# Kernel tuning notes

Measured on AMD Instinct MI355X. Metric: run time of the kernel, lower is better.

Reference implementation:

```python
import jax, jax.numpy as jnp
import numpy as np

NEG_INF = -1e30  # masked_softmax fill (squad util convention)


def setup_inputs() -> dict:
    key = jax.random.key(0)
    ks = jax.random.split(key, 5)
    B, S, H = 4, 2048, 512
    x = jax.random.normal(ks[0], (B, S, H), dtype=jnp.float32)
    mask = jax.random.randint(ks[1], (B, S), 0, 2, dtype=jnp.int32)
    mask = mask.at[:, 0].set(1)  # ensure at least one valid key per row
    W_comb = jax.random.normal(ks[2], (H, 3 * H), dtype=jnp.float32) * (1.0 / np.sqrt(H))
    b_comb = jnp.zeros((3 * H,), dtype=jnp.float32)
    W_out = jax.random.normal(ks[3], (H, H), dtype=jnp.float32) * (1.0 / np.sqrt(H))
    b_out = jnp.zeros((H,), dtype=jnp.float32)
    return {"x": x, "mask": mask, "W_comb": W_comb, "b_comb": b_comb,
            "W_out": W_out, "b_out": b_out}


def reference(x, mask, W_comb, b_comb, W_out, b_out):
    B, S, H = x.shape
    n_head = 8
    d = H // n_head
    scale = d ** 0.5
    qkv = x @ W_comb + b_comb                      # [B,S,3H]
    q, k, v = jnp.split(qkv, 3, axis=-1)
    q = q.reshape(B, S, n_head, d)
    k = k.reshape(B, S, n_head, d)
    v = v.reshape(B, S, n_head, d)
    # [B,h,Sq,Sk] scores; mask applies along the key axis
    scores = jnp.einsum('bqhd,bkhd->bhqk', q / scale, k)
    key_mask = (mask > 0)[:, None, None, :]        # [B,1,1,Sk]
    logits = jnp.where(key_mask, scores, NEG_INF)
    attn = jax.nn.softmax(logits, axis=-1)         # dropout = identity (eval)
    out = jnp.einsum('bhqk,bkhd->bqhd', attn, v).reshape(B, S, H)
    return out @ W_out + b_out
```

## Files before the change

### kernel.cpp

```cpp
#include <hip/hip_runtime.h>
#include <hip/hip_bf16.h>
#include <stdint.h>

typedef unsigned short u16;
typedef unsigned int u32;
typedef __attribute__((ext_vector_type(8))) __bf16 bf16x8;
typedef __attribute__((ext_vector_type(8))) unsigned short us8;
typedef __attribute__((ext_vector_type(4))) unsigned short us4;
typedef __attribute__((ext_vector_type(4))) float f32x4;
typedef __attribute__((ext_vector_type(16))) float f32x16;
typedef __attribute__((ext_vector_type(4))) unsigned int u32x4;
typedef __attribute__((ext_vector_type(2))) unsigned int u32x2;

#define KSCALE_Q 0.18033688011112042f

__device__ inline u16 f2bf(float f) {
  union { __bf16 b; u16 s; } x; x.b = (__bf16)f; return x.s;
}
__device__ inline u32 packbf(float a, float b) {
  return (u32)f2bf(a) | ((u32)f2bf(b) << 16);
}
__device__ inline f32x16 zero16() {
  f32x16 z; for (int i = 0; i < 16; ++i) z[i] = 0.f; return z;
}
__device__ __forceinline__ void gl_lds16(const u16* g, u16* l) {
  __builtin_amdgcn_global_load_lds(
      (const __attribute__((address_space(1))) void*)g,
      (__attribute__((address_space(3))) void*)l, 16, 0, 0);
}
__device__ __forceinline__ void pl32swap(u32& a, u32& b) {
#if __has_builtin(__builtin_amdgcn_permlane32_swap)
  u32x2 r = __builtin_amdgcn_permlane32_swap(a, b, false, false);
  a = r[0]; b = r[1];
#else
  u32 ta = (u32)__shfl_xor((int)a, 32);
  u32 tb = (u32)__shfl_xor((int)b, 32);
  int hi = (threadIdx.x & 63) >> 5;
  u32 na = hi ? tb : a;
  u32 nb = hi ? b : ta;
  a = na; b = nb;
#endif
}

__global__ __launch_bounds__(256) void prep(
    const float* __restrict__ x, const float* __restrict__ Wc,
    const float* __restrict__ Wo, const int* __restrict__ mask,
    u16* __restrict__ xbf, u16* __restrict__ wct, u16* __restrict__ wot,
    int* __restrict__ idx, int* __restrict__ nbv) {
  int r = blockIdx.x, tid = threadIdx.x;
  if (r < 4096) {
    int i = r * 256 + tid;
    float4 v = ((const float4*)x)[i];
    us4 o;
    o[0] = f2bf(v.x); o[1] = f2bf(v.y); o[2] = f2bf(v.z); o[3] = f2bf(v.w);
    ((us4*)xbf)[i] = o;
    return;
  }
  __shared__ float tile[32][33];
  __shared__ int ps[256];
  if (r < 5120) {
    const float* in; u16* outT; int R, C, bi;
    if (r < 4864) { in = Wc; outT = wct; R = 512; C = 1536; bi = r - 4096; }
    else          { in = Wo; outT = wot; R = 512; C = 512;  bi = r - 4864; }
    int nbx = C >> 5;
    int bx = bi % nbx, by = bi / nbx;
    int xq = tid & 31, yq = tid >> 5;
    int c0 = bx * 32, r0 = by * 32;
    for (int j = 0; j < 32; j += 8)
      tile[yq + j][xq] = in[(size_t)(r0 + yq + j) * C + c0 + xq];
    __syncthreads();
    for (int j = 0; j < 32; j += 8)
      outT[(size_t)(c0 + yq + j) * R + r0 + xq] = f2bf(tile[xq][yq + j]);
    return;
  }
  int b = r - 5120;
  const int* mrow = mask + b * 2048;
  int4 a = ((const int4*)mrow)[tid * 2];
  int4 c = ((const int4*)mrow)[tid * 2 + 1];
  int v[8] = {a.x, a.y, a.z, a.w, c.x, c.y, c.z, c.w};
  int cnt = 0;
  for (int i = 0; i < 8; ++i) cnt += (v[i] > 0);
  ps[tid] = cnt;
  __syncthreads();
  for (int off = 1; off < 256; off <<= 1) {
    int xv = ps[tid];
    int yv = (tid >= off) ? ps[tid - off] : 0;
    __syncthreads();
    ps[tid] = xv + yv;
    __syncthreads();
  }
  int total = ps[255];
  int pos = ps[tid] - cnt;
  int* ip = idx + b * 2048;
  for (int i = 0; i < 8; ++i)
    if (v[i] > 0) ip[pos++] = tid * 8 + i;
  for (int i = 0; i < 8; ++i) {
    int j = tid * 8 + i;
    if (j >= total) ip[j] = 0;
  }
  if (tid == 0) nbv[b] = total;
}

__global__ __launch_bounds__(256) void gemm_qkv(
    const u16* __restrict__ A, const u16* __restrict__ Bt,
    const float* __restrict__ bias, u16* __restrict__ Qc,
    u16* __restrict__ Kc, u16* __restrict__ VTc,
    const int* __restrict__ idx, const int* __restrict__ nbv) {
  const int K = 512;
  int bid = blockIdx.x;
  bool isQ = bid < 256;
  int b = 0, m0, n0;
  if (isQ) {
    m0 = (bid >> 2) * 128;
    n0 = (bid & 3) * 128;
  } else {
    int t = bid - 256;
    b = t >> 7;
    int rr_ = t & 127;
    m0 = (rr_ & 15) * 128;
    n0 = (rr_ >> 4) * 128 + 512;
    int npad = (nbv[b] + 127) & ~127;
    if (m0 >= npad) return;
  }
  __shared__ __align__(16) u16 As[128 * 64];
  __shared__ __align__(16) u16 Bs[128 * 64];
  int tid = threadIdx.x, wave = tid >> 6, lane = tid & 63;
  int quad = lane >> 4, l16 = lane & 15;
  int wm = (wave >> 1) * 64, wn = (wave & 1) * 64;

  int r8 = lane >> 3;
  int cb = (lane & 7) ^ r8;
  const u16* agp[4];
  for (int i = 0; i < 4; ++i) {
    int row = m0 + wave * 32 + i * 8 + r8;
    int grow = isQ ? row : (b * 2048 + idx[b * 2048 + row]);
    agp[i] = A + (size_t)grow * K + cb * 8;
  }
  const u16* bg = Bt + (size_t)(n0 + wave * 32 + r8) * K + cb * 8;
  u16* al = As + (wave * 32) * 64 + lane * 8;
  u16* bl = Bs + (wave * 32) * 64 + lane * 8;

  f32x4 acc[4][4];
  for (int i = 0; i < 4; ++i)
    for (int j = 0; j < 4; ++j) acc[i][j] = (f32x4){0.f, 0.f, 0.f, 0.f};

  int rx = l16 & 7;
  for (int kk = 0; kk < K; kk += 64) {
    __syncthreads();
    for (int i = 0; i < 4; ++i)
      gl_lds16(agp[i] + kk, al + i * 8 * 64);
    for (int i = 0; i < 4; ++i)
      gl_lds16(bg + kk + (size_t)(i * 8) * K, bl + i * 8 * 64);
    __syncthreads();
    for (int ks = 0; ks < 2; ++ks) {
      int pos = ((ks * 4 + quad) ^ rx) * 8;
      bf16x8 af[4], bfr[4];
      for (int i = 0; i < 4; ++i)
        af[i] = *(const bf16x8*)(As + (wm + i * 16 + l16) * 64 + pos);
      for (int j = 0; j < 4; ++j)
        bfr[j] = *(const bf16x8*)(Bs + (wn + j * 16 + l16) * 64 + pos);
      for (int i = 0; i < 4; ++i)
        for (int j = 0; j < 4; ++j)
          acc[i][j] = __builtin_amdgcn_mfma_f32_16x16x32_bf16(
              af[i], bfr[j], acc[i][j], 0, 0, 0);
    }
  }
  for (int j = 0; j < 4; ++j) {
    int col = n0 + wn + j * 16 + l16;
    float bv = bias[col];
    if (isQ) {
      for (int i = 0; i < 4; ++i) {
        int rowb = m0 + wm + i * 16 + quad * 4;
        for (int rr = 0; rr < 4; ++rr)
          Qc[(size_t)(rowb + rr) * 512 + col] =
              f2bf((acc[i][j][rr] + bv) * KSCALE_Q);
      }
    } else if (col < 1024) {
      int ck = col - 512;
      for (int i = 0; i < 4; ++i) {
        int key0 = m0 + wm + i * 16 + quad * 4;
        for (int rr = 0; rr < 4; ++rr)
          Kc[((size_t)b * 2048 + key0 + rr) * 512 + ck] =
              f2bf(acc[i][j][rr] + bv);
      }
    } else {
      int hd = col - 1024;
      int h = hd >> 6, d = hd & 63;
      u16* vrow = VTc + ((size_t)(b * 8 + h) * 64 + d) * 2048;
      for (int i = 0; i < 4; ++i) {
        int key0 = m0 + wm + i * 16 + quad * 4;
        us4 pk;
        for (int rr = 0; rr < 4; ++rr) pk[rr] = f2bf(acc[i][j][rr] + bv);
        *(us4*)(vrow + key0) = pk;
      }
    }
  }
}

__global__ __launch_bounds__(256) void gemm_out(
    const u16* __restrict__ A, const u16* __restrict__ Bt,
    const float* __restrict__ bias, float* __restrict__ Cout) {
  const int K = 512, N = 512;
  int m0 = blockIdx.y * 128, n0 = blockIdx.x * 128;
  __shared__ __align__(16) u16 As[128 * 64];
  __shared__ __align__(16) u16 Bs[128 * 64];
  int tid = threadIdx.x, wave = tid >> 6, lane = tid & 63;
  int quad = lane >> 4, l16 = lane & 15;
  int wm = (wave >> 1) * 64, wn = (wave & 1) * 64;

  int r8 = lane >> 3;
  int cb = (lane & 7) ^ r8;
  const u16* ag = A + (size_t)(m0 + wave * 32 + r8) * K + cb * 8;
  const u16* bg = Bt + (size_t)(n0 + wave * 32 + r8) * K + cb * 8;
  u16* al = As + (wave * 32) * 64 + lane * 8;
  u16* bl = Bs + (wave * 32) * 64 + lane * 8;

  f32x4 acc[4][4];
  for (int i = 0; i < 4; ++i)
    for (int j = 0; j < 4; ++j) acc[i][j] = (f32x4){0.f, 0.f, 0.f, 0.f};

  int rx = l16 & 7;
  for (int kk = 0; kk < K; kk += 64) {
    __syncthreads();
    for (int i = 0; i < 4; ++i)
      gl_lds16(ag + kk + (size_t)(i * 8) * K, al + i * 8 * 64);
    for (int i = 0; i < 4; ++i)
      gl_lds16(bg + kk + (size_t)(i * 8) * K, bl + i * 8 * 64);
    __syncthreads();
    for (int ks = 0; ks < 2; ++ks) {
      int pos = ((ks * 4 + quad) ^ rx) * 8;
      bf16x8 af[4], bfr[4];
      for (int i = 0; i < 4; ++i)
        af[i] = *(const bf16x8*)(As + (wm + i * 16 + l16) * 64 + pos);
      for (int j = 0; j < 4; ++j)
        bfr[j] = *(const bf16x8*)(Bs + (wn + j * 16 + l16) * 64 + pos);
      for (int i = 0; i < 4; ++i)
        for (int j = 0; j < 4; ++j)
          acc[i][j] = __builtin_amdgcn_mfma_f32_16x16x32_bf16(
              af[i], bfr[j], acc[i][j], 0, 0, 0);
    }
  }
  for (int j = 0; j < 4; ++j) {
    int col = n0 + wn + j * 16 + l16;
    float bv = bias[col];
    for (int i = 0; i < 4; ++i) {
      int rowb = m0 + wm + i * 16 + quad * 4;
      for (int rr = 0; rr < 4; ++rr)
        Cout[(size_t)(rowb + rr) * N + col] = acc[i][j][rr] + bv;
    }
  }
}

__global__ __launch_bounds__(256) void attn_kernel(
    const u16* __restrict__ Qc, const u16* __restrict__ Kc,
    const u16* __restrict__ VTc, const int* __restrict__ nbv,
    u16* __restrict__ aout) {
  int b = blockIdx.z, h = blockIdx.y, q0 = blockIdx.x * 256;
  int bh = b * 8 + h;
  int tid = threadIdx.x, wave = tid >> 6, lane = tid & 63;
  int l5 = lane & 31, hi = lane >> 5;
  int nb = nbv[b];
  int npad = (nb + 127) & ~127;

  __shared__ __align__(16) u16 Kt[128 * 64];
  __shared__ __align__(16) u16 Vt[64 * 128];

  bf16x8 qf[2][4];
  for (int qg = 0; qg < 2; ++qg) {
    int qrow = b * 2048 + q0 + wave * 64 + qg * 32 + l5;
    for (int s = 0; s < 4; ++s)
      qf[qg][s] = *(const bf16x8*)(Qc + (size_t)qrow * 512 + h * 64 + s * 16 +
                                   hi * 8);
  }

  f32x16 o[2][2];
  for (int qg = 0; qg < 2; ++qg)
    for (int dc = 0; dc < 2; ++dc) o[qg][dc] = zero16();
  float lsum[2] = {0.f, 0.f};

  int krr = lane >> 3;
  int kcb = (lane & 7) ^ krr;
  const u16* kg = Kc + ((size_t)(b * 2048) + wave * 32 + krr) * 512 + h * 64 +
                  kcb * 8;
  u16* kl = Kt + (wave * 32) * 64 + lane * 8;
  int vrr = lane >> 4;
  u16* vl = Vt + (wave * 16) * 128 + lane * 8;

  for (int kt0 = 0; kt0 < npad; kt0 += 128) {
    __syncthreads();
    for (int i = 0; i < 4; ++i)
      gl_lds16(kg + (size_t)(kt0 + i * 8) * 512, kl + i * 8 * 64);
    for (int i = 0; i < 4; ++i) {
      int vr = wave * 16 + i * 4 + vrr;
      int vcb = (lane & 15) ^ (vr & 15);
      gl_lds16(VTc + ((size_t)(bh * 64) + vr) * 2048 + kt0 + vcb * 8,
               vl + i * 4 * 128);
    }
    __syncthreads();

    for (int kg4 = 0; kg4 < 4; ++kg4) {
      int krow = kg4 * 32 + l5;
      const u16* kro = Kt + krow * 64;
      int rx = krow & 7;
      bf16x8 ka[4];
      for (int s = 0; s < 4; ++s)
        ka[s] = *(const bf16x8*)(kro + ((s * 2 + hi) ^ rx) * 8);
      bf16x8 pb[2][2];
      for (int qg = 0; qg < 2; ++qg) {
        f32x16 sa = zero16();
        for (int s = 0; s < 4; ++s)
          sa = __builtin_amdgcn_mfma_f32_32x32x16_bf16(ka[s], qf[qg][s], sa,
                                                       0, 0, 0);
        if (kt0 + 128 > nb) {
          for (int r = 0; r < 16; ++r) {
            int jg = kt0 + kg4 * 32 + (r & 3) + 8 * (r >> 2) + 4 * hi;
            if (jg >= nb) sa[r] = -1e30f;
          }
        }
        u32 pk[8];
        float ls = 0.f;
        for (int j = 0; j < 8; ++j) {
          float e0 = __builtin_amdgcn_exp2f(sa[2 * j]);
          float e1 = __builtin_amdgcn_exp2f(sa[2 * j + 1]);
          ls += e0 + e1;
          pk[j] = packbf(e0, e1);
        }
        lsum[qg] += ls;
        for (int t = 0; t < 2; ++t) {
          u32 a0 = pk[t * 4 + 0], a2 = pk[t * 4 + 2];
          u32 a1 = pk[t * 4 + 1], a3 = pk[t * 4 + 3];
          pl32swap(a0, a2);
          pl32swap(a1, a3);
          u32x4 qv; qv[0] = a0; qv[1] = a1; qv[2] = a2; qv[3] = a3;
          pb[qg][t] = __builtin_bit_cast(bf16x8, qv);
        }
      }
      for (int t = 0; t < 2; ++t) {
        int cblk = kg4 * 4 + t * 2 + hi;
        for (int dc = 0; dc < 2; ++dc) {
          int vrow = dc * 32 + l5;
          bf16x8 va = *(const bf16x8*)(Vt + vrow * 128 +
                                       ((cblk ^ (vrow & 15)) * 8));
          for (int qg = 0; qg < 2; ++qg)
            o[qg][dc] = __builtin_amdgcn_mfma_f32_32x32x16_bf16(
                va, pb[qg][t], o[qg][dc], 0, 0, 0);
        }
      }
    }
  }

  for (int qg = 0; qg < 2; ++qg) {
    float lt = lsum[qg];
    lt += __shfl_xor(lt, 32);
    float inv = 1.f / lt;
    int qrow = b * 2048 + q0 + wave * 64 + qg * 32 + l5;
    for (int dc = 0; dc < 2; ++dc)
      for (int mI = 0; mI < 4; ++mI) {
        us4 pk;
        for (int r = 0; r < 4; ++r) pk[r] = f2bf(o[qg][dc][mI * 4 + r] * inv);
        *(us4*)(aout + (size_t)qrow * 512 + h * 64 + dc * 32 + mI * 8 +
                hi * 4) = pk;
      }
  }
}

extern "C" void kernel_launch(void* const* d_in, const int* in_sizes, int n_in,
                              void* d_out, int out_size, void* d_ws,
                              size_t ws_size, hipStream_t stream) {
  const float* x = (const float*)d_in[0];
  const int* mask = (const int*)d_in[1];
  const float* Wc = (const float*)d_in[2];
  const float* bc = (const float*)d_in[3];
  const float* Wo = (const float*)d_in[4];
  const float* bo = (const float*)d_in[5];
  float* out = (float*)d_out;

  char* ws = (char*)d_ws;
  u16* xbf = (u16*)(ws);
  u16* wct = (u16*)(ws + 8388608);
  u16* wot = (u16*)(ws + 9961472);
  u16* Qc  = (u16*)(ws + 10485760);
  u16* Kc  = (u16*)(ws + 18874368);
  u16* vtc = (u16*)(ws + 27262976);
  int* idx = (int*)(ws + 35651584);
  int* nbv = (int*)(ws + 35684352);
  u16* aout = xbf;

  prep<<<5124, 256, 0, stream>>>(x, Wc, Wo, mask, xbf, wct, wot, idx, nbv);
  gemm_qkv<<<768, 256, 0, stream>>>(xbf, wct, bc, Qc, Kc, vtc, idx, nbv);
  attn_kernel<<<dim3(8, 8, 4), 256, 0, stream>>>(Qc, Kc, vtc, nbv, aout);
  gemm_out<<<dim3(4, 64), 256, 0, stream>>>(aout, wot, bo, out);
}
```

Baseline: 156.4 us.

## Split attention over key range with combine kernel, shrink tiles for more blocks

Attention blocks now cover 128 queries instead of 256 and split the compacted key range into two halves, writing unnormalized fp32 partial outputs and row sums to workspace. A new combine kernel adds the halves, normalizes and writes bf16. The output GEMM tile narrows to 128x64, doubling its grid. This raises the block count to fill more CUs, at the cost of an extra kernel launch, fp32 partial-output traffic, and less K/V reuse per loaded tile.

```diff
diff --git a/kernel.cpp b/kernel.cpp
--- a/kernel.cpp
+++ b/kernel.cpp
@@ -201,46 +201,46 @@
     const u16* __restrict__ A, const u16* __restrict__ Bt,
     const float* __restrict__ bias, float* __restrict__ Cout) {
   const int K = 512, N = 512;
-  int m0 = blockIdx.y * 128, n0 = blockIdx.x * 128;
+  int m0 = blockIdx.y * 128, n0 = blockIdx.x * 64;
   __shared__ __align__(16) u16 As[128 * 64];
-  __shared__ __align__(16) u16 Bs[128 * 64];
+  __shared__ __align__(16) u16 Bs[64 * 64];
   int tid = threadIdx.x, wave = tid >> 6, lane = tid & 63;
   int quad = lane >> 4, l16 = lane & 15;
-  int wm = (wave >> 1) * 64, wn = (wave & 1) * 64;
+  int wm = (wave >> 1) * 64, wn = (wave & 1) * 32;
 
   int r8 = lane >> 3;
   int cb = (lane & 7) ^ r8;
   const u16* ag = A + (size_t)(m0 + wave * 32 + r8) * K + cb * 8;
-  const u16* bg = Bt + (size_t)(n0 + wave * 32 + r8) * K + cb * 8;
+  const u16* bg = Bt + (size_t)(n0 + wave * 16 + r8) * K + cb * 8;
   u16* al = As + (wave * 32) * 64 + lane * 8;
-  u16* bl = Bs + (wave * 32) * 64 + lane * 8;
-
-  f32x4 acc[4][4];
+  u16* bl = Bs + (wave * 16) * 64 + lane * 8;
+
+  f32x4 acc[4][2];
   for (int i = 0; i < 4; ++i)
-    for (int j = 0; j < 4; ++j) acc[i][j] = (f32x4){0.f, 0.f, 0.f, 0.f};
+    for (int j = 0; j < 2; ++j) acc[i][j] = (f32x4){0.f, 0.f, 0.f, 0.f};
 
   int rx = l16 & 7;
   for (int kk = 0; kk < K; kk += 64) {
     __syncthreads();
     for (int i = 0; i < 4; ++i)
       gl_lds16(ag + kk + (size_t)(i * 8) * K, al + i * 8 * 64);
-    for (int i = 0; i < 4; ++i)
+    for (int i = 0; i < 2; ++i)
       gl_lds16(bg + kk + (size_t)(i * 8) * K, bl + i * 8 * 64);
     __syncthreads();
     for (int ks = 0; ks < 2; ++ks) {
       int pos = ((ks * 4 + quad) ^ rx) * 8;
-      bf16x8 af[4], bfr[4];
+      bf16x8 af[4], bfr[2];
       for (int i = 0; i < 4; ++i)
         af[i] = *(const bf16x8*)(As + (wm + i * 16 + l16) * 64 + pos);
-      for (int j = 0; j < 4; ++j)
+      for (int j = 0; j < 2; ++j)
         bfr[j] = *(const bf16x8*)(Bs + (wn + j * 16 + l16) * 64 + pos);
       for (int i = 0; i < 4; ++i)
-        for (int j = 0; j < 4; ++j)
+        for (int j = 0; j < 2; ++j)
           acc[i][j] = __builtin_amdgcn_mfma_f32_16x16x32_bf16(
               af[i], bfr[j], acc[i][j], 0, 0, 0);
     }
   }
-  for (int j = 0; j < 4; ++j) {
+  for (int j = 0; j < 2; ++j) {
     int col = n0 + wn + j * 16 + l16;
     float bv = bias[col];
     for (int i = 0; i < 4; ++i) {
@@ -254,29 +254,30 @@
 __global__ __launch_bounds__(256) void attn_kernel(
     const u16* __restrict__ Qc, const u16* __restrict__ Kc,
     const u16* __restrict__ VTc, const int* __restrict__ nbv,
-    u16* __restrict__ aout) {
-  int b = blockIdx.z, h = blockIdx.y, q0 = blockIdx.x * 256;
+    float* __restrict__ Op, float* __restrict__ lp) {
+  int zz = blockIdx.z;
+  int b = zz >> 1, sp = zz & 1;
+  int h = blockIdx.y, q0 = blockIdx.x * 128;
   int bh = b * 8 + h;
   int tid = threadIdx.x, wave = tid >> 6, lane = tid & 63;
   int l5 = lane & 31, hi = lane >> 5;
   int nb = nbv[b];
   int npad = (nb + 127) & ~127;
+  int tiles = npad >> 7;
+  int t0 = (tiles + 1) >> 1;
+  int ktA = sp ? t0 * 128 : 0;
+  int ktB = sp ? npad : t0 * 128;
 
   __shared__ __align__(16) u16 Kt[128 * 64];
   __shared__ __align__(16) u16 Vt[64 * 128];
 
-  bf16x8 qf[2][4];
-  for (int qg = 0; qg < 2; ++qg) {
-    int qrow = b * 2048 + q0 + wave * 64 + qg * 32 + l5;
-    for (int s = 0; s < 4; ++s)
-      qf[qg][s] = *(const bf16x8*)(Qc + (size_t)qrow * 512 + h * 64 + s * 16 +
-                                   hi * 8);
-  }
-
-  f32x16 o[2][2];
-  for (int qg = 0; qg < 2; ++qg)
-    for (int dc = 0; dc < 2; ++dc) o[qg][dc] = zero16();
-  float lsum[2] = {0.f, 0.f};
+  int qrow = b * 2048 + q0 + wave * 32 + l5;
+  bf16x8 qf[4];
+  for (int s = 0; s < 4; ++s)
+    qf[s] = *(const bf16x8*)(Qc + (size_t)qrow * 512 + h * 64 + s * 16 + hi * 8);
+
+  f32x16 o0 = zero16(), o1 = zero16();
+  float lsum = 0.f;
 
   int krr = lane >> 3;
   int kcb = (lane & 7) ^ krr;
@@ -286,7 +287,7 @@
   int vrr = lane >> 4;
   u16* vl = Vt + (wave * 16) * 128 + lane * 8;
 
-  for (int kt0 = 0; kt0 < npad; kt0 += 128) {
+  for (int kt0 = ktA; kt0 < ktB; kt0 += 128) {
     __syncthreads();
     for (int i = 0; i < 4; ++i)
       gl_lds16(kg + (size_t)(kt0 + i * 8) * 512, kl + i * 8 * 64);
@@ -302,65 +303,82 @@
       int krow = kg4 * 32 + l5;
       const u16* kro = Kt + krow * 64;
       int rx = krow & 7;
-      bf16x8 ka[4];
-      for (int s = 0; s < 4; ++s)
-        ka[s] = *(const bf16x8*)(kro + ((s * 2 + hi) ^ rx) * 8);
-      bf16x8 pb[2][2];
-      for (int qg = 0; qg < 2; ++qg) {
-        f32x16 sa = zero16();
-        for (int s = 0; s < 4; ++s)
-          sa = __builtin_amdgcn_mfma_f32_32x32x16_bf16(ka[s], qf[qg][s], sa,
-                                                       0, 0, 0);
-        if (kt0 + 128 > nb) {
-          for (int r = 0; r < 16; ++r) {
-            int jg = kt0 + kg4 * 32 + (r & 3) + 8 * (r >> 2) + 4 * hi;
-            if (jg >= nb) sa[r] = -1e30f;
-          }
+      f32x16 sa = zero16();
+      for (int s = 0; s < 4; ++s) {
+        bf16x8 ka = *(const bf16x8*)(kro + ((s * 2 + hi) ^ rx) * 8);
+        sa = __builtin_amdgcn_mfma_f32_32x32x16_bf16(ka, qf[s], sa, 0, 0, 0);
+      }
+      if (kt0 + 128 > nb) {
+        for (int r = 0; r < 16; ++r) {
+          int jg = kt0 + kg4 * 32 + (r & 3) + 8 * (r >> 2) + 4 * hi;
+          if (jg >= nb) sa[r] = -1e30f;
         }
-        u32 pk[8];
-        float ls = 0.f;
-        for (int j = 0; j < 8; ++j) {
-          float e0 = __builtin_amdgcn_exp2f(sa[2 * j]);
-          float e1 = __builtin_amdgcn_exp2f(sa[2 * j + 1]);
-          ls += e0 + e1;
-          pk[j] = packbf(e0, e1);
-        }
-        lsum[qg] += ls;
-        for (int t = 0; t < 2; ++t) {
-          u32 a0 = pk[t * 4 + 0], a2 = pk[t * 4 + 2];
-          u32 a1 = pk[t * 4 + 1], a3 = pk[t * 4 + 3];
-          pl32swap(a0, a2);
-          pl32swap(a1, a3);
-          u32x4 qv; qv[0] = a0; qv[1] = a1; qv[2] = a2; qv[3] = a3;
-          pb[qg][t] = __builtin_bit_cast(bf16x8, qv);
-        }
+      }
+      u32 pk[8];
+      for (int j = 0; j < 8; ++j) {
+        float e0 = __builtin_amdgcn_exp2f(sa[2 * j]);
+        float e1 = __builtin_amdgcn_exp2f(sa[2 * j + 1]);
+        lsum += e0 + e1;
+        pk[j] = packbf(e0, e1);
       }
       for (int t = 0; t < 2; ++t) {
+        u32 a0 = pk[t * 4 + 0], a2 = pk[t * 4 + 2];
+        u32 a1 = pk[t * 4 + 1], a3 = pk[t * 4 + 3];
+        pl32swap(a0, a2);
+        pl32swap(a1, a3);
+        u32x4 qv; qv[0] = a0; qv[1] = a1; qv[2] = a2; qv[3] = a3;
+        bf16x8 pb = __builtin_bit_cast(bf16x8, qv);
         int cblk = kg4 * 4 + t * 2 + hi;
-        for (int dc = 0; dc < 2; ++dc) {
-          int vrow = dc * 32 + l5;
+        {
+          int vrow = l5;
           bf16x8 va = *(const bf16x8*)(Vt + vrow * 128 +
                                        ((cblk ^ (vrow & 15)) * 8));
-          for (int qg = 0; qg < 2; ++qg)
-            o[qg][dc] = __builtin_amdgcn_mfma_f32_32x32x16_bf16(
-                va, pb[qg][t], o[qg][dc], 0, 0, 0);
+          o0 = __builtin_amdgcn_mfma_f32_32x32x16_bf16(va, pb, o0, 0, 0, 0);
         }
-      }
-    }
-  }
-
-  for (int qg = 0; qg < 2; ++qg) {
-    float lt = lsum[qg];
-    lt += __shfl_xor(lt, 32);
-    float inv = 1.f / lt;
-    int qrow = b * 2048 + q0 + wave * 64 + qg * 32 + l5;
-    for (int dc = 0; dc < 2; ++dc)
-      for (int mI = 0; mI < 4; ++mI) {
-        us4 pk;
-        for (int r = 0; r < 4; ++r) pk[r] = f2bf(o[qg][dc][mI * 4 + r] * inv);
-        *(us4*)(aout + (size_t)qrow * 512 + h * 64 + dc * 32 + mI * 8 +
-                hi * 4) = pk;
-      }
+        {
+          int vrow = 32 + l5;
+          bf16x8 va = *(const bf16x8*)(Vt + vrow * 128 +
+                                       ((cblk ^ (vrow & 15)) * 8));
+          o1 = __builtin_amdgcn_mfma_f32_32x32x16_bf16(va, pb, o1, 0, 0, 0);
+        }
+      }
+    }
+  }
+
+  lsum += __shfl_xor(lsum, 32);
+  if (hi == 0) lp[(size_t)sp * 65536 + (size_t)qrow * 8 + h] = lsum;
+  float* ob = Op + (size_t)sp * 4194304 + (size_t)qrow * 512 + h * 64;
+  f32x16 oo[2]; oo[0] = o0; oo[1] = o1;
+  for (int dc = 0; dc < 2; ++dc)
+    for (int mI = 0; mI < 4; ++mI) {
+      float4 v;
+      v.x = oo[dc][mI * 4 + 0]; v.y = oo[dc][mI * 4 + 1];
+      v.z = oo[dc][mI * 4 + 2]; v.w = oo[dc][mI * 4 + 3];
+      *(float4*)(ob + dc * 32 + mI * 8 + hi * 4) = v;
+    }
+}
+
+__global__ __launch_bounds__(256) void combine(
+    const float* __restrict__ Op, const float* __restrict__ lp,
+    u16* __restrict__ aout) {
+  int r = blockIdx.x * 16 + (threadIdx.x >> 4);
+  int c4 = (threadIdx.x & 15) * 4;
+  const float* o0 = Op + (size_t)r * 512;
+  const float* o1 = o0 + 4194304;
+  const float* l0 = lp + (size_t)r * 8;
+  const float* l1 = l0 + 65536;
+  u16* ao = aout + (size_t)r * 512;
+  for (int j = 0; j < 8; ++j) {
+    float inv = 1.f / (l0[j] + l1[j]);
+    int c = j * 64 + c4;
+    float4 a = *(const float4*)(o0 + c);
+    float4 b2 = *(const float4*)(o1 + c);
+    us4 pk;
+    pk[0] = f2bf((a.x + b2.x) * inv);
+    pk[1] = f2bf((a.y + b2.y) * inv);
+    pk[2] = f2bf((a.z + b2.z) * inv);
+    pk[3] = f2bf((a.w + b2.w) * inv);
+    *(us4*)(ao + c) = pk;
   }
 }
 
@@ -384,10 +402,13 @@
   u16* vtc = (u16*)(ws + 27262976);
   int* idx = (int*)(ws + 35651584);
   int* nbv = (int*)(ws + 35684352);
+  float* Op = (float*)(ws + 37748736);
+  float* lp = (float*)(ws + 71303168);
   u16* aout = xbf;
 
   prep<<<5124, 256, 0, stream>>>(x, Wc, Wo, mask, xbf, wct, wot, idx, nbv);
   gemm_qkv<<<768, 256, 0, stream>>>(xbf, wct, bc, Qc, Kc, vtc, idx, nbv);
-  attn_kernel<<<dim3(8, 8, 4), 256, 0, stream>>>(Qc, Kc, vtc, nbv, aout);
-  gemm_out<<<dim3(4, 64), 256, 0, stream>>>(aout, wot, bo, out);
-}
+  attn_kernel<<<dim3(16, 8, 8), 256, 0, stream>>>(Qc, Kc, vtc, nbv, Op, lp);
+  combine<<<512, 256, 0, stream>>>(Op, lp, aout);
+  gemm_out<<<dim3(8, 64), 256, 0, stream>>>(aout, wot, bo, out);
+}
```

New measurement: 158.0 us. Within noise of the previous version (+1.0%).
